# Optimization experiments

Hardware: AMD Instinct MI355X
Metric: run time of the kernel (lower is better)

The kernel has to match this reference:

```python
import jax, jax.numpy as jnp
import numpy as np

NUM_BINS = 64
Z_MIN, Z_MAX = -3.0, 1.0
BIN_SIZE = (Z_MAX - Z_MIN) / NUM_BINS
EPS_MEAN = 1e-5
EPS_BN = 1e-5


def setup_inputs() -> dict:
    key = jax.random.key(0)
    k1, k2, k3, k4 = jax.random.split(key, 4)
    M, N, C = 100000, 64, 4
    feat_channels, out_dim = 64, NUM_BINS * 3
    features = jax.random.normal(k1, (M, N, C), dtype=jnp.float32)
    num_points = jax.random.randint(k2, (M,), 0, 65, dtype=jnp.int32)
    coors = jax.random.randint(k3, (M, 4), 0, 100, dtype=jnp.int32)
    W = jax.random.normal(k4, (feat_channels, out_dim), dtype=jnp.float32) * (1.0 / np.sqrt(out_dim))
    b = jnp.zeros((feat_channels,), dtype=jnp.float32)
    gamma = jnp.ones((feat_channels,), dtype=jnp.float32)
    beta = jnp.zeros((feat_channels,), dtype=jnp.float32)
    return {"features": features, "num_points": num_points, "coors": coors,
            "W": W, "b": b, "gamma": gamma, "beta": beta}


def reference(features, num_points, coors, W, b, gamma, beta):
    M, N, C = features.shape
    # validity mask per point
    mask = (jnp.arange(N)[None, :] < num_points[:, None]).astype(features.dtype)  # [M, N]
    z = features[..., 2]  # [M, N]
    r = features[..., 3]  # [M, N]
    bin_idx = jnp.clip(((z - Z_MIN) / BIN_SIZE).astype(jnp.int32), 0, NUM_BINS - 1)  # [M, N]

    rows = jnp.arange(M)[:, None]  # [M, 1] broadcast against [M, N]
    zeros = jnp.zeros((M, NUM_BINS), dtype=features.dtype)
    count = zeros.at[rows, bin_idx].add(mask)
    sum_z = zeros.at[rows, bin_idx].add(z * mask)
    sum_r = zeros.at[rows, bin_idx].add(r * mask)
    mean_z = sum_z / (count + EPS_MEAN)
    mean_r = sum_r / (count + EPS_MEAN)

    # interleaved layout [count, mean_z, mean_r] per bin -> [M, 3*NUM_BINS]
    hist = jnp.stack([count, mean_z, mean_r], axis=-1).reshape(M, NUM_BINS * 3)

    # Linear -> BatchNorm1d (training: biased batch stats) -> ReLU
    x = hist @ W.T + b  # [M, feat_channels]
    mu = jnp.mean(x, axis=0)
    var = jnp.mean((x - mu) ** 2, axis=0)
    xn = (x - mu) / jnp.sqrt(var + EPS_BN)
    return jax.nn.relu(xn * gamma + beta)
```

## Files before the change

kernel.cpp:

```cpp
#include <hip/hip_runtime.h>
#include <hip/hip_bf16.h>
#include <math.h>


typedef __attribute__((ext_vector_type(8))) short bf16x8;
typedef __attribute__((ext_vector_type(4))) float f32x4;
typedef __attribute__((ext_vector_type(4))) int   i32x4;

#define ZMINF   (-3.0f)
#define INV_BIN 16.0f
#define QS      8192.0f
#define INV_QS  (1.0f / 8192.0f)
#define PBIASF  65536.0f
#define PBIASI  65536
#define CBIT    16777216
#define TSC     16777216.0f
#define INV_TSC (1.0f / 16777216.0f)
#define REPS    16

__device__ __forceinline__ short f2bf(float f) {
    __hip_bfloat16 h = __float2bfloat16(f);
    return __builtin_bit_cast(short, h);
}

__global__ __launch_bounds__(256)
void k0_prep(const float* __restrict__ W,
             short*       __restrict__ wsW,
             unsigned long long* __restrict__ totals)
{
    const int tid    = blockIdx.x * 256 + threadIdx.x;
    const int stride = gridDim.x * 256;
    for (int e = tid; e < 24 * 64 * 8; e += stride) {
        const int j  = e & 7;
        const int ln = (e >> 3) & 63;
        const int st = e >> 9;
        const int s  = st >> 2, t = st & 3;
        const int k  = s * 32 + (ln >> 4) * 8 + j;
        const int n  = t * 16 + (ln & 15);
        const int wc = (k < 64) ? 3 * k
                     : (k < 128) ? 3 * (k - 64) + 1
                                 : 3 * (k - 128) + 2;
        wsW[e] = f2bf(W[n * 192 + wc]);
    }
    for (int e = tid; e < REPS * 128; e += stride) totals[e] = 0ull;
}

__global__ __launch_bounds__(256, 8)
void k1_hist_mfma(const uint2*  __restrict__ feat2,
                  const int*    __restrict__ nump,
                  const bf16x8* __restrict__ wsWf,
                  const float*  __restrict__ bvec,
                  float*        __restrict__ xout,
                  unsigned long long* __restrict__ totals,
                  int M)
{
    __shared__ int sH[2 * 16 * 128];

    const int tid  = threadIdx.x;
    const int wave = tid >> 6;
    const int lane = tid & 63;
    const int col  = lane & 15;
    const int quad = lane >> 4;
    const int pair = wave >> 1;
    const int half = wave & 1;

    const int gbase = blockIdx.x * 32 + pair * 16;
    int* hp = &sH[pair * 2048];

    float psum[2] = {0.f, 0.f};
    float psq[2]  = {0.f, 0.f};
    bf16x8 bcur[2];

    if (gbase < M) {
        uint2 zw[8];
        const int npv = nump[min(gbase + half * 8 + (lane & 7), M - 1)];
        #pragma unroll
        for (int uu = 0; uu < 8; ++uu) {
            const int rc = min(gbase + half * 8 + uu, M - 1);
            zw[uu] = feat2[((size_t)rc * 64 + lane) * 2 + 1];
        }

        {
            i32x4* p4 = (i32x4*)(hp + half * 1024);
            #pragma unroll
            for (int i = 0; i < 4; ++i) p4[lane + i * 64] = i32x4{0, 0, 0, 0};
        }
        __builtin_amdgcn_wave_barrier();

        #pragma unroll
        for (int uu = 0; uu < 8; ++uu) {
            const int u = half * 8 + uu;
            int np_u = __builtin_amdgcn_readlane(npv, uu);
            np_u = (gbase + u < M) ? np_u : 0;
            if (lane < np_u) {
                const float z  = __int_as_float((int)zw[uu].x);
                const float rr = __int_as_float((int)zw[uu].y);
                int bi = (int)((z - ZMINF) * INV_BIN);
                bi = min(max(bi, 0), 63);
                const int sw = (bi + u * 4) & 63;
                int* hrow = hp + u * 128;
                atomicAdd(hrow + sw,      CBIT + PBIASI + (int)(z * QS));
                atomicAdd(hrow + 64 + sw, PBIASI + (int)(rr * QS));
            }
        }

        #pragma unroll
        for (int tt = 0; tt < 2; ++tt)
            bcur[tt] = wsWf[(half * 2 + tt) * 64 + lane];
    }

    __syncthreads();

    if (gbase < M) {
        f32x4 acc[2] = {};
        bf16x8 bnxt[2];
        const int* ar  = hp + col * 128;
        const int  rot = col * 4;
        int   z0[8], z1[8];
        float cnt0[8], cnt1[8], rcp0[8], rcp1[8];
        #pragma unroll
        for (int s = 0; s < 6; ++s) {
            if (s < 5) {
                #pragma unroll
                for (int tt = 0; tt < 2; ++tt)
                    bnxt[tt] = wsWf[((s + 1) * 4 + half * 2 + tt) * 64 + lane];
            }
            float av[8];
            if (s == 0 || s == 1) {
                const int o0 = (s * 32 + quad * 8 + rot) & 63;
                const int o1 = (s * 32 + quad * 8 + 4 + rot) & 63;
                const i32x4 a0 = *(const i32x4*)(ar + o0);
                const i32x4 a1 = *(const i32x4*)(ar + o1);
                int* zc = (s == 0) ? z0 : z1;
                float* cc = (s == 0) ? cnt0 : cnt1;
                zc[0]=a0.x; zc[1]=a0.y; zc[2]=a0.z; zc[3]=a0.w;
                zc[4]=a1.x; zc[5]=a1.y; zc[6]=a1.z; zc[7]=a1.w;
                #pragma unroll
                for (int j = 0; j < 8; ++j) { cc[j] = (float)(zc[j] >> 24); av[j] = cc[j]; }
            } else if (s == 2 || s == 3) {
                const int*   zc = (s == 2) ? z0 : z1;
                const float* cc = (s == 2) ? cnt0 : cnt1;
                float* rp = (s == 2) ? rcp0 : rcp1;
                #pragma unroll
                for (int j = 0; j < 8; ++j) {
                    rp[j] = __builtin_amdgcn_rcpf(cc[j] + 1e-5f) * INV_QS;
                    const float pay = (float)(zc[j] & 0xFFFFFF);
                    av[j] = (pay - cc[j] * PBIASF) * rp[j];
                }
            } else {
                const int o0 = ((s - 4) * 32 + quad * 8 + rot) & 63;
                const int o1 = ((s - 4) * 32 + quad * 8 + 4 + rot) & 63;
                const i32x4 a0 = *(const i32x4*)(ar + 64 + o0);
                const i32x4 a1 = *(const i32x4*)(ar + 64 + o1);
                const int rv[8] = {a0.x, a0.y, a0.z, a0.w, a1.x, a1.y, a1.z, a1.w};
                const float* cc = (s == 4) ? cnt0 : cnt1;
                const float* rp = (s == 4) ? rcp0 : rcp1;
                #pragma unroll
                for (int j = 0; j < 8; ++j)
                    av[j] = ((float)rv[j] - cc[j] * PBIASF) * rp[j];
            }
            bf16x8 af;
            #pragma unroll
            for (int j = 0; j < 8; ++j) af[j] = f2bf(av[j]);
            #pragma unroll
            for (int tt = 0; tt < 2; ++tt)
                acc[tt] = __builtin_amdgcn_mfma_f32_16x16x32_bf16(af, bcur[tt], acc[tt], 0, 0, 0);
            #pragma unroll
            for (int tt = 0; tt < 2; ++tt) bcur[tt] = bnxt[tt];
        }

        #pragma unroll
        for (int tt = 0; tt < 2; ++tt) {
            const int t = half * 2 + tt;
            const float bias = bvec[t * 16 + col];
            #pragma unroll
            for (int i = 0; i < 4; ++i) {
                const int row = gbase + quad * 4 + i;
                if (row < M) {
                    const float xv = acc[tt][i] + bias;
                    xout[(size_t)row * 64 + t * 16 + col] = xv;
                    psum[tt] += xv;
                    psq[tt]  += xv * xv;
                }
            }
        }
    }

    #pragma unroll
    for (int tt = 0; tt < 2; ++tt) {
        psum[tt] += __shfl_xor(psum[tt], 16);
        psum[tt] += __shfl_xor(psum[tt], 32);
        psq[tt]  += __shfl_xor(psq[tt], 16);
        psq[tt]  += __shfl_xor(psq[tt], 32);
    }
    const float myS = (quad & 1) ? psum[1] : psum[0];
    const float myQ = (quad & 1) ? psq[1]  : psq[0];
    const int gw = blockIdx.x * 4 + wave;
    if (lane < 32) {
        unsigned long long* dst = totals + (gw & (REPS - 1)) * 128 + half * 32 + lane;
        atomicAdd(dst,      (unsigned long long)(long long)(myS * TSC));
        atomicAdd(dst + 64, (unsigned long long)(long long)(myQ * TSC));
    }
}

__global__ __launch_bounds__(256)
void k3_bn_apply(float4* __restrict__ x,
                 const unsigned long long* __restrict__ totals,
                 const float* __restrict__ gamma,
                 const float* __restrict__ beta,
                 float invM, int n4)
{
    __shared__ float sT[128];
    __shared__ float sa[64];
    __shared__ float sc[64];
    const int t = threadIdx.x;
    if (t < 128) {
        long long s = 0;
        #pragma unroll
        for (int rep = 0; rep < REPS; ++rep) s += (long long)totals[rep * 128 + t];
        sT[t] = (float)s * (invM * INV_TSC);
    }
    __syncthreads();
    if (t < 64) {
        const float mu   = sT[t];
        const float q    = sT[64 + t];
        const float var  = q - mu * mu;
        const float rstd = 1.0f / sqrtf(var + 1e-5f);
        const float a    = gamma[t] * rstd;
        sa[t] = a;
        sc[t] = beta[t] - mu * a;
    }
    __syncthreads();
    const int stride = gridDim.x * 256;
    for (int i = blockIdx.x * 256 + t; i < n4; i += stride) {
        const float4 a = ((const float4*)sa)[i & 15];
        const float4 c = ((const float4*)sc)[i & 15];
        float4 v = x[i];
        v.x = fmaxf(fmaf(v.x, a.x, c.x), 0.f);
        v.y = fmaxf(fmaf(v.y, a.y, c.y), 0.f);
        v.z = fmaxf(fmaf(v.z, a.z, c.z), 0.f);
        v.w = fmaxf(fmaf(v.w, a.w, c.w), 0.f);
        x[i] = v;
    }
}

extern "C" void kernel_launch(void* const* d_in, const int* in_sizes, int n_in,
                              void* d_out, int out_size, void* d_ws, size_t ws_size,
                              hipStream_t stream) {
    const uint2*  feat2 = (const uint2*)d_in[0];
    const int*    nump  = (const int*)d_in[1];
    const float*  W     = (const float*)d_in[3];
    const float*  bvec  = (const float*)d_in[4];
    const float*  gamma = (const float*)d_in[5];
    const float*  beta  = (const float*)d_in[6];

    const int M = in_sizes[1];
    float* xout = (float*)d_out;
    short* wsW  = (short*)d_ws;
    unsigned long long* totals =
        (unsigned long long*)((char*)d_ws + 24 * 64 * 8 * sizeof(short));

    k0_prep<<<16, 256, 0, stream>>>(W, wsW, totals);

    const int nblk = (M + 31) / 32;
    k1_hist_mfma<<<nblk, 256, 0, stream>>>(feat2, nump, (const bf16x8*)wsW, bvec, xout, totals, M);

    const int n4 = out_size / 4;
    const int nblk3 = (n4 + 256 * 16 - 1) / (256 * 16);
    k3_bn_apply<<<nblk3, 256, 0, stream>>>((float4*)d_out, totals, gamma, beta,
                                           1.0f / (float)M, n4);
}
```

Measured before the change: 193.2 us.

## Pack z and r histogram accumulators into 64-bit LDS atomics with padded rows

Each histogram bin now holds a 64-bit word: the count-plus-z payload in the high half and the r payload in the low half. One 64-bit LDS atomic per point replaces two 32-bit atomics, rows are padded to stride 66 instead of rotated, and the MFMA A-operand read fetches both halves with one set of vector loads. Blocks shrink from 256 to 128 threads, one 16-row tile each, and the MFMA loop is reordered to reuse the count and reciprocal values. The risks are 64-bit atomic throughput in LDS, possible bank conflicts with the new stride, and carry from the low half into the high half if the r sum ever went negative.

```diff
diff --git a/kernel.cpp b/kernel.cpp
--- a/kernel.cpp
+++ b/kernel.cpp
@@ -17,6 +17,7 @@
 #define TSC     16777216.0f
 #define INV_TSC (1.0f / 16777216.0f)
 #define REPS    16
+#define RSTRIDE 66
 
 __device__ __forceinline__ short f2bf(float f) {
     __hip_bfloat16 h = __float2bfloat16(f);
@@ -45,7 +46,7 @@
     for (int e = tid; e < REPS * 128; e += stride) totals[e] = 0ull;
 }
 
-__global__ __launch_bounds__(256, 8)
+__global__ __launch_bounds__(128, 8)
 void k1_hist_mfma(const uint2*  __restrict__ feat2,
                   const int*    __restrict__ nump,
                   const bf16x8* __restrict__ wsWf,
@@ -54,19 +55,16 @@
                   unsigned long long* __restrict__ totals,
                   int M)
 {
-    __shared__ int sH[2 * 16 * 128];
+    __shared__ unsigned long long sH[16 * RSTRIDE];
 
     const int tid  = threadIdx.x;
     const int wave = tid >> 6;
     const int lane = tid & 63;
     const int col  = lane & 15;
     const int quad = lane >> 4;
-    const int pair = wave >> 1;
-    const int half = wave & 1;
-
-    const int gbase = blockIdx.x * 32 + pair * 16;
-    int* hp = &sH[pair * 2048];
-
+    const int half = wave;
+
+    const int gbase = blockIdx.x * 16;
     float psum[2] = {0.f, 0.f};
     float psq[2]  = {0.f, 0.f};
     bf16x8 bcur[2];
@@ -81,9 +79,12 @@
         }
 
         {
-            i32x4* p4 = (i32x4*)(hp + half * 1024);
-            #pragma unroll
-            for (int i = 0; i < 4; ++i) p4[lane + i * 64] = i32x4{0, 0, 0, 0};
+            i32x4* p4 = (i32x4*)&sH[(size_t)half * 8 * RSTRIDE];
+            #pragma unroll
+            for (int i = 0; i < 5; ++i) {
+                const int idx = lane + i * 64;
+                if (idx < (8 * RSTRIDE * 2) / 4) p4[idx] = i32x4{0, 0, 0, 0};
+            }
         }
         __builtin_amdgcn_wave_barrier();
 
@@ -97,16 +98,15 @@
                 const float rr = __int_as_float((int)zw[uu].y);
                 int bi = (int)((z - ZMINF) * INV_BIN);
                 bi = min(max(bi, 0), 63);
-                const int sw = (bi + u * 4) & 63;
-                int* hrow = hp + u * 128;
-                atomicAdd(hrow + sw,      CBIT + PBIASI + (int)(z * QS));
-                atomicAdd(hrow + 64 + sw, PBIASI + (int)(rr * QS));
-            }
-        }
-
-        #pragma unroll
-        for (int tt = 0; tt < 2; ++tt)
-            bcur[tt] = wsWf[(half * 2 + tt) * 64 + lane];
+                const unsigned long long add =
+                    ((unsigned long long)(unsigned)(CBIT + PBIASI + (int)(z * QS)) << 32)
+                    | (unsigned)(PBIASI + (int)(rr * QS));
+                atomicAdd(&sH[u * RSTRIDE + bi], add);
+            }
+        }
+
+        bcur[0] = wsWf[(half * 2 + 0) * 64 + lane];
+        bcur[1] = wsWf[(half * 2 + 1) * 64 + lane];
     }
 
     __syncthreads();
@@ -114,59 +114,53 @@
     if (gbase < M) {
         f32x4 acc[2] = {};
         bf16x8 bnxt[2];
-        const int* ar  = hp + col * 128;
-        const int  rot = col * 4;
-        int   z0[8], z1[8];
-        float cnt0[8], cnt1[8], rcp0[8], rcp1[8];
-        #pragma unroll
-        for (int s = 0; s < 6; ++s) {
-            if (s < 5) {
-                #pragma unroll
-                for (int tt = 0; tt < 2; ++tt)
-                    bnxt[tt] = wsWf[((s + 1) * 4 + half * 2 + tt) * 64 + lane];
-            }
-            float av[8];
-            if (s == 0 || s == 1) {
-                const int o0 = (s * 32 + quad * 8 + rot) & 63;
-                const int o1 = (s * 32 + quad * 8 + 4 + rot) & 63;
-                const i32x4 a0 = *(const i32x4*)(ar + o0);
-                const i32x4 a1 = *(const i32x4*)(ar + o1);
-                int* zc = (s == 0) ? z0 : z1;
-                float* cc = (s == 0) ? cnt0 : cnt1;
-                zc[0]=a0.x; zc[1]=a0.y; zc[2]=a0.z; zc[3]=a0.w;
-                zc[4]=a1.x; zc[5]=a1.y; zc[6]=a1.z; zc[7]=a1.w;
-                #pragma unroll
-                for (int j = 0; j < 8; ++j) { cc[j] = (float)(zc[j] >> 24); av[j] = cc[j]; }
-            } else if (s == 2 || s == 3) {
-                const int*   zc = (s == 2) ? z0 : z1;
-                const float* cc = (s == 2) ? cnt0 : cnt1;
-                float* rp = (s == 2) ? rcp0 : rcp1;
-                #pragma unroll
-                for (int j = 0; j < 8; ++j) {
-                    rp[j] = __builtin_amdgcn_rcpf(cc[j] + 1e-5f) * INV_QS;
-                    const float pay = (float)(zc[j] & 0xFFFFFF);
-                    av[j] = (pay - cc[j] * PBIASF) * rp[j];
-                }
-            } else {
-                const int o0 = ((s - 4) * 32 + quad * 8 + rot) & 63;
-                const int o1 = ((s - 4) * 32 + quad * 8 + 4 + rot) & 63;
-                const i32x4 a0 = *(const i32x4*)(ar + 64 + o0);
-                const i32x4 a1 = *(const i32x4*)(ar + 64 + o1);
-                const int rv[8] = {a0.x, a0.y, a0.z, a0.w, a1.x, a1.y, a1.z, a1.w};
-                const float* cc = (s == 4) ? cnt0 : cnt1;
-                const float* rp = (s == 4) ? rcp0 : rcp1;
-                #pragma unroll
-                for (int j = 0; j < 8; ++j)
-                    av[j] = ((float)rv[j] - cc[j] * PBIASF) * rp[j];
-            }
+        const int* ar = (const int*)sH + col * (RSTRIDE * 2);
+        #pragma unroll
+        for (int g = 0; g < 2; ++g) {
+            const int o0 = g * 32 + quad * 8;
+            const i32x4* ap = (const i32x4*)(ar + 2 * o0);
+            const i32x4 a0 = ap[0], a1 = ap[1], a2 = ap[2], a3 = ap[3];
+            const int zz[8]  = {a0.y, a0.w, a1.y, a1.w, a2.y, a2.w, a3.y, a3.w};
+            const int rrw[8] = {a0.x, a0.z, a1.x, a1.z, a2.x, a2.z, a3.x, a3.z};
+            float cnt[8], rcp[8], av[8];
             bf16x8 af;
+
+            bnxt[0] = wsWf[((2 + g) * 4 + half * 2 + 0) * 64 + lane];
+            bnxt[1] = wsWf[((2 + g) * 4 + half * 2 + 1) * 64 + lane];
+            #pragma unroll
+            for (int j = 0; j < 8; ++j) { cnt[j] = (float)(zz[j] >> 24); av[j] = cnt[j]; }
             #pragma unroll
             for (int j = 0; j < 8; ++j) af[j] = f2bf(av[j]);
-            #pragma unroll
-            for (int tt = 0; tt < 2; ++tt)
-                acc[tt] = __builtin_amdgcn_mfma_f32_16x16x32_bf16(af, bcur[tt], acc[tt], 0, 0, 0);
-            #pragma unroll
-            for (int tt = 0; tt < 2; ++tt) bcur[tt] = bnxt[tt];
+            acc[0] = __builtin_amdgcn_mfma_f32_16x16x32_bf16(af, bcur[0], acc[0], 0, 0, 0);
+            acc[1] = __builtin_amdgcn_mfma_f32_16x16x32_bf16(af, bcur[1], acc[1], 0, 0, 0);
+            bcur[0] = bnxt[0]; bcur[1] = bnxt[1];
+
+            bnxt[0] = wsWf[((4 + g) * 4 + half * 2 + 0) * 64 + lane];
+            bnxt[1] = wsWf[((4 + g) * 4 + half * 2 + 1) * 64 + lane];
+            #pragma unroll
+            for (int j = 0; j < 8; ++j) {
+                rcp[j] = __builtin_amdgcn_rcpf(cnt[j] + 1e-5f) * INV_QS;
+                const float pay = (float)(zz[j] & 0xFFFFFF);
+                av[j] = (pay - cnt[j] * PBIASF) * rcp[j];
+            }
+            #pragma unroll
+            for (int j = 0; j < 8; ++j) af[j] = f2bf(av[j]);
+            acc[0] = __builtin_amdgcn_mfma_f32_16x16x32_bf16(af, bcur[0], acc[0], 0, 0, 0);
+            acc[1] = __builtin_amdgcn_mfma_f32_16x16x32_bf16(af, bcur[1], acc[1], 0, 0, 0);
+            bcur[0] = bnxt[0]; bcur[1] = bnxt[1];
+
+            if (g == 0) {
+                bnxt[0] = wsWf[(1 * 4 + half * 2 + 0) * 64 + lane];
+                bnxt[1] = wsWf[(1 * 4 + half * 2 + 1) * 64 + lane];
+            }
+            #pragma unroll
+            for (int j = 0; j < 8; ++j)
+                av[j] = ((float)rrw[j] - cnt[j] * PBIASF) * rcp[j];
+            #pragma unroll
+            for (int j = 0; j < 8; ++j) af[j] = f2bf(av[j]);
+            acc[0] = __builtin_amdgcn_mfma_f32_16x16x32_bf16(af, bcur[0], acc[0], 0, 0, 0);
+            acc[1] = __builtin_amdgcn_mfma_f32_16x16x32_bf16(af, bcur[1], acc[1], 0, 0, 0);
+            bcur[0] = bnxt[0]; bcur[1] = bnxt[1];
         }
 
         #pragma unroll
@@ -195,7 +189,7 @@
     }
     const float myS = (quad & 1) ? psum[1] : psum[0];
     const float myQ = (quad & 1) ? psq[1]  : psq[0];
-    const int gw = blockIdx.x * 4 + wave;
+    const int gw = blockIdx.x * 2 + wave;
     if (lane < 32) {
         unsigned long long* dst = totals + (gw & (REPS - 1)) * 128 + half * 32 + lane;
         atomicAdd(dst,      (unsigned long long)(long long)(myS * TSC));
@@ -262,8 +256,8 @@
 
     k0_prep<<<16, 256, 0, stream>>>(W, wsW, totals);
 
-    const int nblk = (M + 31) / 32;
-    k1_hist_mfma<<<nblk, 256, 0, stream>>>(feat2, nump, (const bf16x8*)wsW, bvec, xout, totals, M);
+    const int nblk = (M + 15) / 16;
+    k1_hist_mfma<<<nblk, 128, 0, stream>>>(feat2, nump, (const bf16x8*)wsW, bvec, xout, totals, M);
 
     const int n4 = out_size / 4;
     const int nblk3 = (n4 + 256 * 16 - 1) / (256 * 16);
```

After: 185.0 us. 1.04x faster.
